# Optimization experiments

Hardware: AMD Instinct MI355X
Metric: run time of the kernel (lower is better)

Reference implementation:

```python
import jax, jax.numpy as jnp
import numpy as np

N, D, H, K, C = 8192, 1024, 512, 16, 9  # patches, embed, hidden, heads, classes


def setup_inputs() -> dict:
    key = jax.random.key(0)
    ks = jax.random.split(key, 20)
    sD = 1.0 / np.sqrt(D)
    sH = 1.0 / np.sqrt(H)
    inp = {
        "x": jax.random.normal(ks[0], (N, D), jnp.float32),
        # gated attention heads, stacked over K heads; weights stored [in, out]
        "Vw": jax.random.normal(ks[1], (K, D, H), jnp.float32) * sD,
        "Vb": jax.random.normal(ks[2], (K, H), jnp.float32) * sD,
        "Uw": jax.random.normal(ks[3], (K, D, H), jnp.float32) * sD,
        "Ub": jax.random.normal(ks[4], (K, H), jnp.float32) * sD,
        "ww": jax.random.normal(ks[5], (K, H), jnp.float32) * sH,
        "wb": jax.random.normal(ks[6], (K,), jnp.float32) * sH,
        # average-pooling head MLP: D -> H -> D
        "pW1": jax.random.normal(ks[7], (D, H), jnp.float32) * sD,
        "pb1": jax.random.normal(ks[8], (H,), jnp.float32) * sD,
        "pW2": jax.random.normal(ks[9], (H, D), jnp.float32) * sH,
        "pb2": jax.random.normal(ks[10], (D,), jnp.float32) * sH,
        # classifier: D -> 1024 -> 512 -> 256 -> C
        "cW1": jax.random.normal(ks[11], (D, 1024), jnp.float32) * sD,
        "cb1": jax.random.normal(ks[12], (1024,), jnp.float32) * sD,
        "cW2": jax.random.normal(ks[13], (1024, 512), jnp.float32) * (1.0 / np.sqrt(1024)),
        "cb2": jax.random.normal(ks[14], (512,), jnp.float32) * (1.0 / np.sqrt(1024)),
        "cW3": jax.random.normal(ks[15], (512, 256), jnp.float32) * (1.0 / np.sqrt(512)),
        "cb3": jax.random.normal(ks[16], (256,), jnp.float32) * (1.0 / np.sqrt(512)),
        "cW4": jax.random.normal(ks[17], (256, C), jnp.float32) * (1.0 / np.sqrt(256)),
        "cb4": jax.random.normal(ks[18], (C,), jnp.float32) * (1.0 / np.sqrt(256)),
    }
    return inp


def reference(x, Vw, Vb, Uw, Ub, ww, wb, pW1, pb1, pW2, pb2,
              cW1, cb1, cW2, cb2, cW3, cb3, cW4, cb4):
    # --- multi-head gated attention (all K heads batched) ---
    AV = jnp.tanh(jnp.einsum('nd,kdh->knh', x, Vw) + Vb[:, None, :])          # [K,N,H]
    AU = jax.nn.sigmoid(jnp.einsum('nd,kdh->knh', x, Uw) + Ub[:, None, :])    # [K,N,H]
    scores = jnp.einsum('knh,kh->kn', AV * AU, ww) + wb[:, None]              # [K,N]
    A = jax.nn.softmax(scores, axis=1)                                        # softmax over patches
    agg_heads = jnp.einsum('kn,nd->kd', A, x)                                 # [K,D]
    # --- average pooling head: mean over patches then MLP D->H->D ---
    m = jnp.mean(x, axis=0)
    avg_agg = jax.nn.relu(m @ pW1 + pb1) @ pW2 + pb2                          # [D]
    # --- mean over all K+1 heads ---
    aggregated = (jnp.sum(agg_heads, axis=0) + avg_agg) / (K + 1)             # [D]
    # --- classifier (eval mode: dropout = identity) ---
    h = jax.nn.relu(aggregated @ cW1 + cb1)
    h = jax.nn.relu(h @ cW2 + cb2)
    h = jax.nn.relu(h @ cW3 + cb3)
    logits = h @ cW4 + cb4                                                    # [C]
    # eval mode applies softmax (not self.training branch)
    return jax.nn.softmax(logits, axis=-1)
```

## Files before the change

### kernel.cpp

```cpp
#include <hip/hip_runtime.h>
#include <stdint.h>

#define N_PATCH 8192
#define DIM     1024
#define HID     512
#define NHEAD   16

using i32x4 = __attribute__((ext_vector_type(4))) int;

__device__ __forceinline__ void gload_lds16(const void* g, void* l) {
  __builtin_amdgcn_global_load_lds(
      reinterpret_cast<const __attribute__((address_space(1))) void*>(
          reinterpret_cast<uintptr_t>(g)),
      reinterpret_cast<__attribute__((address_space(3))) void*>(
          reinterpret_cast<uintptr_t>(l)),
      16, 0, 0);
}

__device__ __forceinline__ int q8(float v, float rs) {
  int q = (int)rintf(v * rs);
  return q > 127 ? 127 : (q < -127 ? -127 : q);
}

__global__ void prep1_kernel(const float* __restrict__ x,
                             signed char* __restrict__ xq, float* __restrict__ sx,
                             const float* __restrict__ Vw, const float* __restrict__ Uw,
                             float* __restrict__ swp, float* __restrict__ rswp) {
  __shared__ __align__(16) float red4[16][16][4];
  const int bid = blockIdx.x;
  const int t = threadIdx.x;
  if (bid < 2048) {
    const int row = bid * 4 + (t >> 6);
    const int lane = t & 63;
    const float* xr = x + (size_t)row * DIM;
    float4 v[4];
    float am = 0.f;
    #pragma unroll
    for (int j = 0; j < 4; ++j) {
      v[j] = *(const float4*)&xr[j * 256 + lane * 4];
      am = fmaxf(am, fmaxf(fmaxf(fabsf(v[j].x), fabsf(v[j].y)),
                           fmaxf(fabsf(v[j].z), fabsf(v[j].w))));
    }
    #pragma unroll
    for (int s = 32; s; s >>= 1) am = fmaxf(am, __shfl_xor(am, s, 64));
    const float rs = (am > 0.f) ? 127.f / am : 0.f;
    #pragma unroll
    for (int j = 0; j < 4; ++j) {
      int b = (q8(v[j].x, rs) & 255) | ((q8(v[j].y, rs) & 255) << 8) |
              ((q8(v[j].z, rs) & 255) << 16) | ((q8(v[j].w, rs) & 255) << 24);
      ((int*)xq)[row * 256 + j * 64 + lane] = b;
    }
    if (lane == 0) sx[row] = am / 127.f;
    return;
  }
  const int b2 = bid - 2048;
  const int u = b2 >> 7, k = (b2 >> 3) & 15, hc = b2 & 7;
  const float* W = u ? Uw : Vw;
  const int h4 = t & 15, dseg = t >> 4;
  const size_t base = (size_t)k * DIM * HID + hc * 64 + h4 * 4;
  float4 am4 = {0.f, 0.f, 0.f, 0.f};
  for (int i = 0; i < 64; ++i) {
    float4 v = *(const float4*)&W[base + (size_t)(dseg * 64 + i) * HID];
    am4.x = fmaxf(am4.x, fabsf(v.x));
    am4.y = fmaxf(am4.y, fabsf(v.y));
    am4.z = fmaxf(am4.z, fabsf(v.z));
    am4.w = fmaxf(am4.w, fabsf(v.w));
  }
  *(float4*)&red4[dseg][h4][0] = am4;
  __syncthreads();
  if (t < 64) {
    float m = 0.f;
    #pragma unroll
    for (int ds = 0; ds < 16; ++ds) m = fmaxf(m, red4[ds][t >> 2][t & 3]);
    const int h = hc * 64 + t;
    const int c = (h >> 4) * 32 + u * 16 + (h & 15);
    swp[k * 1024 + c]  = m / 127.f;
    rswp[k * 1024 + c] = (m > 0.f) ? 127.f / m : 0.f;
  }
}

__global__ void pack_wq_kernel(const float* __restrict__ Vw,
                               const float* __restrict__ Uw,
                               const float* __restrict__ rswp,
                               signed char* __restrict__ Wq) {
  __shared__ __align__(16) signed char T[128][80];
  const int bid = blockIdx.x;
  const int k = bid >> 7, hc = (bid >> 4) & 7, dc = bid & 15;
  const int t = threadIdx.x;
  const int d0 = dc * 64, h0 = hc * 64;
  const int hh = t & 63;
  const size_t base = (size_t)k * DIM * HID;
  #pragma unroll
  for (int u = 0; u < 2; ++u) {
    const float* W = u ? Uw : Vw;
    const int h = h0 + hh;
    const int cl = ((hh >> 4) << 5) + (u << 4) + (hh & 15);
    const float rs = rswp[k * 1024 + hc * 128 + cl];
    #pragma unroll
    for (int i = 0; i < 16; ++i) {
      const int dd = i * 4 + (t >> 6);
      T[cl][dd] = (signed char)q8(W[base + (size_t)(d0 + dd) * HID + h], rs);
    }
  }
  __syncthreads();
  #pragma unroll
  for (int j = 0; j < 2; ++j) {
    const int idx = j * 256 + t;
    const int cl = idx >> 2, dq = idx & 3;
    i32x4 val = *(const i32x4*)&T[cl][dq * 16];
    const size_t col = (size_t)k * 1024 + hc * 128 + cl;
    *(i32x4*)&Wq[col * DIM + d0 + dq * 16] = val;
  }
}

__global__ __launch_bounds__(512, 1) void gemm_scores_kernel(
    const signed char* __restrict__ xq, const signed char* __restrict__ Wq,
    const float* __restrict__ sx, const float* __restrict__ swp,
    const float* __restrict__ Vb, const float* __restrict__ Ub,
    const float* __restrict__ ww, float* __restrict__ part) {
  __shared__ __align__(16) signed char As[2][32768];
  __shared__ __align__(16) signed char Bs[2][32768];
  const int bid = blockIdx.x;
  const int x8 = bid & 7;
  const int s  = (bid >> 3) & 31;
  const int w  = bid >> 8;
  const int mt = (x8 & 1) * 16 + (w & 1) * 8 + (s >> 2);
  const int ct = (x8 >> 1) * 16 + (w >> 1) * 4 + (s & 3);
  const int kh = ct >> 2, cb = ct & 3;
  const int tid = threadIdx.x;
  const int wv = tid >> 6, lane = tid & 63;
  const int wr = wv >> 2, wc = wv & 3;
  const int l15 = lane & 15, l4 = lane >> 4;

  const signed char* Ab = xq + (size_t)mt * 256 * DIM;
  const signed char* Bb = Wq + (size_t)ct * 256 * DIM;

  i32x4 acc[8][4];
  #pragma unroll
  for (int i = 0; i < 8; ++i)
    #pragma unroll
    for (int j = 0; j < 4; ++j) acc[i][j] = (i32x4){0, 0, 0, 0};

  auto stageA_h = [&](int t, int half) {
    const int buf = t & 1, db = t << 7;
    #pragma unroll
    for (int pp = 0; pp < 2; ++pp) {
      const int p = half * 2 + pp;
      const int r = p * 64 + (tid >> 3);
      const int ksrc = ((tid & 7) * 16) ^ (((r >> 1) & 7) << 4);
      gload_lds16(Ab + (size_t)r * DIM + db + ksrc,
                  (char*)&As[buf][0] + p * 8192 + wv * 1024);
    }
  };
  auto stageB_h = [&](int t, int half) {
    const int buf = t & 1, db = t << 7;
    #pragma unroll
    for (int pp = 0; pp < 2; ++pp) {
      const int p = half * 2 + pp;
      const int r = p * 64 + (tid >> 3);
      const int ksrc = ((tid & 7) * 16) ^ (((r >> 1) & 7) << 4);
      gload_lds16(Bb + (size_t)r * DIM + db + ksrc,
                  (char*)&Bs[buf][0] + p * 8192 + wv * 1024);
    }
  };

  const int swz = ((l15 >> 1) & 7) << 4;
  const int kb0 = (0 * 64 + l4 * 16) ^ swz;
  const int kb1 = (1 * 64 + l4 * 16) ^ swz;
  const int aRow = (wr * 128 + l15) * 128;
  const int bRow = (wc * 64 + l15) * 128;

  i32x4 a[8], b[4], a2[8], b2[4];

  stageA_h(0, 0); stageA_h(0, 1); stageB_h(0, 0); stageB_h(0, 1);
  stageA_h(1, 0); stageA_h(1, 1); stageB_h(1, 0); stageB_h(1, 1);
  __syncthreads();

  for (int u = 0; u < 8; ++u) {
    const int buf = u & 1;
    const char* Abase = (const char*)&As[buf][0];
    const char* Bbase = (const char*)&Bs[buf][0];
    #pragma unroll
    for (int f = 0; f < 8; ++f) a[f] = *(const i32x4*)(Abase + aRow + f * 2048 + kb0);
    #pragma unroll
    for (int nf = 0; nf < 4; ++nf) b[nf] = *(const i32x4*)(Bbase + bRow + nf * 2048 + kb0);
    if (u < 7) { stageA_h(u + 1, 0); stageB_h(u + 1, 0); }
    #pragma unroll
    for (int f = 0; f < 8; ++f) a2[f] = *(const i32x4*)(Abase + aRow + f * 2048 + kb1);
    #pragma unroll
    for (int nf = 0; nf < 4; ++nf) b2[nf] = *(const i32x4*)(Bbase + bRow + nf * 2048 + kb1);
    __builtin_amdgcn_s_setprio(1);
    #pragma unroll
    for (int f = 0; f < 8; ++f)
      #pragma unroll
      for (int nf = 0; nf < 4; ++nf)
        acc[f][nf] = __builtin_amdgcn_mfma_i32_16x16x64_i8(a[f], b[nf], acc[f][nf], 0, 0, 0);
    __builtin_amdgcn_s_setprio(0);
    if (u < 7) { stageA_h(u + 1, 1); stageB_h(u + 1, 1); }
    __builtin_amdgcn_s_setprio(1);
    #pragma unroll
    for (int f = 0; f < 8; ++f)
      #pragma unroll
      for (int nf = 0; nf < 4; ++nf)
        acc[f][nf] = __builtin_amdgcn_mfma_i32_16x16x64_i8(a2[f], b2[nf], acc[f][nf], 0, 0, 0);
    __builtin_amdgcn_s_setprio(0);
    __syncthreads();
  }

  float partial[8][4];
  #pragma unroll
  for (int f = 0; f < 8; ++f)
    #pragma unroll
    for (int r = 0; r < 4; ++r) partial[f][r] = 0.f;

  float vb[2], ub[2], wwv[2], swv[2], swu[2];
  #pragma unroll
  for (int p = 0; p < 2; ++p) {
    const int hl = (cb * 8 + wc * 2 + p) * 16 + l15;
    vb[p]  = Vb[kh * HID + hl];
    ub[p]  = Ub[kh * HID + hl];
    wwv[p] = ww[kh * HID + hl];
    swv[p] = swp[ct * 256 + wc * 64 + (2 * p) * 16 + l15];
    swu[p] = swp[ct * 256 + wc * 64 + (2 * p + 1) * 16 + l15];
  }
  const int rbase = mt * 256 + wr * 128 + l4 * 4;
  #pragma unroll
  for (int f = 0; f < 8; ++f) {
    const float4 sx4 = *(const float4*)&sx[rbase + f * 16];
    const float sxr[4] = {sx4.x, sx4.y, sx4.z, sx4.w};
    #pragma unroll
    for (int p = 0; p < 2; ++p)
      #pragma unroll
      for (int r = 0; r < 4; ++r) {
        const float scv = (float)acc[f][2 * p][r] * (sxr[r] * swv[p]) + vb[p];
        const float scu = (float)acc[f][2 * p + 1][r] * (sxr[r] * swu[p]) + ub[p];
        const float e2 = __expf(2.f * scv);
        const float av = 1.f - 2.f / (e2 + 1.f);
        const float au = 1.f / (1.f + __expf(-scu));
        partial[f][r] += av * au * wwv[p];
      }
  }
  #pragma unroll
  for (int s2 = 1; s2 < 16; s2 <<= 1)
    #pragma unroll
    for (int f = 0; f < 8; ++f)
      #pragma unroll
      for (int r = 0; r < 4; ++r)
        partial[f][r] += __shfl_xor(partial[f][r], s2, 64);

  float* red = (float*)&As[0][0];
  if (l15 == 0) {
    #pragma unroll
    for (int f = 0; f < 8; ++f)
      #pragma unroll
      for (int r = 0; r < 4; ++r)
        red[(wr * 4 + wc) * 128 + f * 16 + l4 * 4 + r] = partial[f][r];
  }
  __syncthreads();
  if (tid < 256) {
    const int row = tid;
    const int wr2 = row >> 7, lr = row & 127;
    const float* rp = red + wr2 * 4 * 128;
    const float v = rp[lr] + rp[128 + lr] + rp[256 + lr] + rp[384 + lr];
    part[((size_t)cb * NHEAD + kh) * N_PATCH + mt * 256 + row] = v;
  }
}

__global__ void scores_part_kernel(const float* __restrict__ part,
                                   float* __restrict__ scores,
                                   float* __restrict__ spart) {
  const int k = blockIdx.x >> 3, c = blockIdx.x & 7;
  const int t = threadIdx.x;
  __shared__ float shm[4], shs[4];
  float v[4];
  float mx = -1e30f;
  #pragma unroll
  for (int i = 0; i < 4; ++i) {
    const int n = c * 1024 + i * 256 + t;
    float s = 0.f;
    #pragma unroll
    for (int j = 0; j < 4; ++j) s += part[((size_t)j * NHEAD + k) * N_PATCH + n];
    v[i] = s;
    scores[(size_t)k * N_PATCH + n] = s;
    mx = fmaxf(mx, s);
  }
  #pragma unroll
  for (int sft = 32; sft; sft >>= 1) mx = fmaxf(mx, __shfl_xor(mx, sft, 64));
  const int wv = t >> 6;
  if ((t & 63) == 0) shm[wv] = mx;
  __syncthreads();
  mx = fmaxf(fmaxf(shm[0], shm[1]), fmaxf(shm[2], shm[3]));
  float sum = 0.f;
  #pragma unroll
  for (int i = 0; i < 4; ++i) sum += __expf(v[i] - mx);
  #pragma unroll
  for (int sft = 32; sft; sft >>= 1) sum += __shfl_xor(sum, sft, 64);
  if ((t & 63) == 0) shs[wv] = sum;
  __syncthreads();
  if (t == 0) {
    spart[(k * 8 + c) * 2]     = mx;
    spart[(k * 8 + c) * 2 + 1] = shs[0] + shs[1] + shs[2] + shs[3];
  }
}

__global__ void weighted_part_kernel(const signed char* __restrict__ xq,
                                     const float* __restrict__ sx,
                                     const float* __restrict__ scores,
                                     const float* __restrict__ spart,
                                     float* __restrict__ wp1,
                                     float* __restrict__ wp2) {
  __shared__ float wsx[128], s2x[128];
  __shared__ float sm[16], srz[16];
  const int d = blockIdx.x * 256 + threadIdx.x;
  const int nc = blockIdx.y;
  if (threadIdx.x < 16) {
    const int k = threadIdx.x;
    float m = -1e30f;
    #pragma unroll
    for (int c = 0; c < 8; ++c) m = fmaxf(m, spart[(k * 8 + c) * 2]);
    float S = 0.f;
    #pragma unroll
    for (int c = 0; c < 8; ++c)
      S += spart[(k * 8 + c) * 2 + 1] * __expf(spart[(k * 8 + c) * 2] - m);
    sm[k] = m; srz[k] = 1.f / S;
  }
  __syncthreads();
  if (threadIdx.x < 128) {
    const int n = nc * 128 + threadIdx.x;
    float s = 0.f;
    #pragma unroll
    for (int k = 0; k < NHEAD; ++k)
      s += __expf(scores[(size_t)k * N_PATCH + n] - sm[k]) * srz[k];
    const float sxn = sx[n];
    wsx[threadIdx.x] = s * sxn;
    s2x[threadIdx.x] = sxn;
  }
  __syncthreads();
  float a1 = 0.f, a2 = 0.f;
  for (int i = 0; i < 128; ++i) {
    const float q = (float)xq[(size_t)(nc * 128 + i) * DIM + d];
    a1 += wsx[i] * q;
    a2 += s2x[i] * q;
  }
  wp1[nc * DIM + d] = a1;
  wp2[nc * DIM + d] = a2;
}

__global__ void reduce_vec_kernel(const float* __restrict__ wp1,
                                  const float* __restrict__ wp2,
                                  float* __restrict__ y1,
                                  float* __restrict__ mvec) {
  int d = blockIdx.x * 256 + threadIdx.x;
  float s1 = 0.f, s2 = 0.f;
  #pragma unroll
  for (int i = 0; i < 64; ++i) {
    s1 += wp1[i * DIM + d];
    s2 += wp2[i * DIM + d];
  }
  y1[d] = s1;
  mvec[d] = s2 * (1.f / (float)N_PATCH);
}

__global__ void gemv_fused_kernel(const float* __restrict__ in,
                                  const float* __restrict__ W,
                                  const float* __restrict__ bias,
                                  const float* __restrict__ extra, float scale,
                                  int do_relu, float* __restrict__ out,
                                  int In, int Out) {
  __shared__ float red[4][64];
  const int jl = threadIdx.x & 63, kc = threadIdx.x >> 6;
  const int j = blockIdx.x * 64 + jl;
  const int chunk = In >> 2;
  const float* Wp = W + (size_t)(kc * chunk) * Out + j;
  const float* ip = in + kc * chunk;
  float acc = 0.f;
  #pragma unroll 4
  for (int d = 0; d < chunk; ++d) acc += ip[d] * Wp[(size_t)d * Out];
  if (kc) red[kc][jl] = acc;
  __syncthreads();
  if (kc == 0) {
    float v = bias[j] + acc + red[1][jl] + red[2][jl] + red[3][jl];
    if (extra) v += extra[j];
    v *= scale;
    if (do_relu) v = fmaxf(v, 0.f);
    out[j] = v;
  }
}

__global__ void c3_final_kernel(const float* __restrict__ c2,
                                const float* __restrict__ W3,
                                const float* __restrict__ b3,
                                const float* __restrict__ W4,
                                const float* __restrict__ b4,
                                float* __restrict__ out) {
  __shared__ float c3s[256];
  __shared__ float logits[9];
  const int t = threadIdx.x;
  float acc = b3[t];
  #pragma unroll 4
  for (int d = 0; d < 512; ++d) acc += c2[d] * W3[(size_t)d * 256 + t];
  c3s[t] = fmaxf(acc, 0.f);
  __syncthreads();
  if (t < 9) {
    float l = b4[t];
    for (int d = 0; d < 256; ++d) l += c3s[d] * W4[d * 9 + t];
    logits[t] = l;
  }
  __syncthreads();
  if (t == 0) {
    float mx = logits[0];
    for (int j = 1; j < 9; ++j) mx = fmaxf(mx, logits[j]);
    float e[9], s = 0.f;
    for (int j = 0; j < 9; ++j) { e[j] = expf(logits[j] - mx); s += e[j]; }
    for (int j = 0; j < 9; ++j) out[j] = e[j] / s;
  }
}

extern "C" void kernel_launch(void* const* d_in, const int* in_sizes, int n_in,
                              void* d_out, int out_size, void* d_ws, size_t ws_size,
                              hipStream_t stream) {
  (void)in_sizes; (void)n_in; (void)out_size; (void)ws_size;
  const float* x   = (const float*)d_in[0];
  const float* Vw  = (const float*)d_in[1];
  const float* Vb  = (const float*)d_in[2];
  const float* Uw  = (const float*)d_in[3];
  const float* Ub  = (const float*)d_in[4];
  const float* ww  = (const float*)d_in[5];
  const float* pW1 = (const float*)d_in[7];
  const float* pb1 = (const float*)d_in[8];
  const float* pW2 = (const float*)d_in[9];
  const float* pb2 = (const float*)d_in[10];
  const float* cW1 = (const float*)d_in[11];
  const float* cb1 = (const float*)d_in[12];
  const float* cW2 = (const float*)d_in[13];
  const float* cb2 = (const float*)d_in[14];
  const float* cW3 = (const float*)d_in[15];
  const float* cb3 = (const float*)d_in[16];
  const float* cW4 = (const float*)d_in[17];
  const float* cb4 = (const float*)d_in[18];
  float* out = (float*)d_out;

  char* ws = (char*)d_ws;
  size_t o = 0;
  auto alloc = [&](size_t bytes) -> char* {
    char* p = ws + o;
    o += (bytes + 255) & ~(size_t)255;
    return p;
  };
  signed char* xq = (signed char*)alloc((size_t)N_PATCH * DIM);
  signed char* Wq = (signed char*)alloc((size_t)NHEAD * 1024 * DIM);
  float* sx    = (float*)alloc(N_PATCH * 4);
  float* swp   = (float*)alloc(NHEAD * 1024 * 4);
  float* rswp  = (float*)alloc(NHEAD * 1024 * 4);
  float* part  = (float*)alloc((size_t)4 * NHEAD * N_PATCH * 4);
  float* scores= (float*)alloc((size_t)NHEAD * N_PATCH * 4);
  float* spart = (float*)alloc(NHEAD * 8 * 2 * 4);
  float* wp1   = (float*)alloc(64 * DIM * 4);
  float* wp2   = (float*)alloc(64 * DIM * 4);
  float* y1    = (float*)alloc(DIM * 4);
  float* mvec  = (float*)alloc(DIM * 4);
  float* h1    = (float*)alloc(HID * 4);
  float* aggr  = (float*)alloc(DIM * 4);
  float* c1    = (float*)alloc(1024 * 4);
  float* c2    = (float*)alloc(512 * 4);

  prep1_kernel<<<2304, 256, 0, stream>>>(x, xq, sx, Vw, Uw, swp, rswp);
  pack_wq_kernel<<<2048, 256, 0, stream>>>(Vw, Uw, rswp, Wq);
  gemm_scores_kernel<<<2048, 512, 0, stream>>>(xq, Wq, sx, swp, Vb, Ub, ww, part);
  scores_part_kernel<<<128, 256, 0, stream>>>(part, scores, spart);
  weighted_part_kernel<<<dim3(4, 64), 256, 0, stream>>>(xq, sx, scores, spart, wp1, wp2);
  reduce_vec_kernel<<<4, 256, 0, stream>>>(wp1, wp2, y1, mvec);
  gemv_fused_kernel<<<8, 256, 0, stream>>>(mvec, pW1, pb1, nullptr, 1.f, 1, h1, DIM, HID);
  gemv_fused_kernel<<<16, 256, 0, stream>>>(h1, pW2, pb2, y1, 1.f / 17.f, 0, aggr, HID, DIM);
  gemv_fused_kernel<<<16, 256, 0, stream>>>(aggr, cW1, cb1, nullptr, 1.f, 1, c1, 1024, 1024);
  gemv_fused_kernel<<<8, 256, 0, stream>>>(c1, cW2, cb2, nullptr, 1.f, 1, c2, 1024, 512);
  c3_final_kernel<<<1, 256, 0, stream>>>(c2, cW3, cb3, cW4, cb4, out);
}
```

Measured before the change: 371.4 us.

## Fuse weight absmax reduction into pack kernel and vectorize weight quantization

The per-column absmax scale computation for Vw/Uw moves out of prep1 and into pack_wq, so each block computes its own scales, keeps the reciprocals in shared memory and then quantizes and transposes the weights. This drops the rswp buffer and the dependency across kernels on it, and pack_wq now reads weights with float4 loads instead of scalar loads. The grid shrinks from 2048 to 256 blocks, each doing more work (re-reading its weight slice twice). That lowers parallelism for the packing step and adds more syncthreads per block.

```diff
diff --git a/kernel.cpp b/kernel.cpp
--- a/kernel.cpp
+++ b/kernel.cpp
@@ -23,93 +23,91 @@
 }
 
 __global__ void prep1_kernel(const float* __restrict__ x,
-                             signed char* __restrict__ xq, float* __restrict__ sx,
-                             const float* __restrict__ Vw, const float* __restrict__ Uw,
-                             float* __restrict__ swp, float* __restrict__ rswp) {
-  __shared__ __align__(16) float red4[16][16][4];
+                             signed char* __restrict__ xq, float* __restrict__ sx) {
   const int bid = blockIdx.x;
   const int t = threadIdx.x;
-  if (bid < 2048) {
-    const int row = bid * 4 + (t >> 6);
-    const int lane = t & 63;
-    const float* xr = x + (size_t)row * DIM;
-    float4 v[4];
-    float am = 0.f;
-    #pragma unroll
-    for (int j = 0; j < 4; ++j) {
-      v[j] = *(const float4*)&xr[j * 256 + lane * 4];
-      am = fmaxf(am, fmaxf(fmaxf(fabsf(v[j].x), fabsf(v[j].y)),
-                           fmaxf(fabsf(v[j].z), fabsf(v[j].w))));
+  const int row = bid * 4 + (t >> 6);
+  const int lane = t & 63;
+  const float* xr = x + (size_t)row * DIM;
+  float4 v[4];
+  float am = 0.f;
+  #pragma unroll
+  for (int j = 0; j < 4; ++j) {
+    v[j] = *(const float4*)&xr[j * 256 + lane * 4];
+    am = fmaxf(am, fmaxf(fmaxf(fabsf(v[j].x), fabsf(v[j].y)),
+                         fmaxf(fabsf(v[j].z), fabsf(v[j].w))));
+  }
+  #pragma unroll
+  for (int s = 32; s; s >>= 1) am = fmaxf(am, __shfl_xor(am, s, 64));
+  const float rs = (am > 0.f) ? 127.f / am : 0.f;
+  #pragma unroll
+  for (int j = 0; j < 4; ++j) {
+    int b = (q8(v[j].x, rs) & 255) | ((q8(v[j].y, rs) & 255) << 8) |
+            ((q8(v[j].z, rs) & 255) << 16) | ((q8(v[j].w, rs) & 255) << 24);
+    ((int*)xq)[row * 256 + j * 64 + lane] = b;
+  }
+  if (lane == 0) sx[row] = am / 127.f;
+}
+
+__global__ void pack_wq_kernel(const float* __restrict__ Vw,
+                               const float* __restrict__ Uw,
+                               float* __restrict__ swp,
+                               signed char* __restrict__ Wq) {
+  __shared__ __align__(16) float redm[16][64];
+  __shared__ float rsL[64];
+  __shared__ __align__(16) signed char T[64][288];
+  const int bid = blockIdx.x;
+  const int u = bid >> 7, k = (bid >> 3) & 15, hc = bid & 7;
+  const float* W = u ? Uw : Vw;
+  const int t = threadIdx.x;
+  const size_t base = (size_t)k * DIM * HID + hc * 64;
+
+  {
+    const int h4 = t & 15, dseg = t >> 4;
+    float4 am4 = {0.f, 0.f, 0.f, 0.f};
+    for (int i = 0; i < 64; ++i) {
+      float4 v = *(const float4*)&W[base + (size_t)(dseg * 64 + i) * HID + h4 * 4];
+      am4.x = fmaxf(am4.x, fabsf(v.x));
+      am4.y = fmaxf(am4.y, fabsf(v.y));
+      am4.z = fmaxf(am4.z, fabsf(v.z));
+      am4.w = fmaxf(am4.w, fabsf(v.w));
     }
-    #pragma unroll
-    for (int s = 32; s; s >>= 1) am = fmaxf(am, __shfl_xor(am, s, 64));
-    const float rs = (am > 0.f) ? 127.f / am : 0.f;
-    #pragma unroll
-    for (int j = 0; j < 4; ++j) {
-      int b = (q8(v[j].x, rs) & 255) | ((q8(v[j].y, rs) & 255) << 8) |
-              ((q8(v[j].z, rs) & 255) << 16) | ((q8(v[j].w, rs) & 255) << 24);
-      ((int*)xq)[row * 256 + j * 64 + lane] = b;
-    }
-    if (lane == 0) sx[row] = am / 127.f;
-    return;
-  }
-  const int b2 = bid - 2048;
-  const int u = b2 >> 7, k = (b2 >> 3) & 15, hc = b2 & 7;
-  const float* W = u ? Uw : Vw;
-  const int h4 = t & 15, dseg = t >> 4;
-  const size_t base = (size_t)k * DIM * HID + hc * 64 + h4 * 4;
-  float4 am4 = {0.f, 0.f, 0.f, 0.f};
-  for (int i = 0; i < 64; ++i) {
-    float4 v = *(const float4*)&W[base + (size_t)(dseg * 64 + i) * HID];
-    am4.x = fmaxf(am4.x, fabsf(v.x));
-    am4.y = fmaxf(am4.y, fabsf(v.y));
-    am4.z = fmaxf(am4.z, fabsf(v.z));
-    am4.w = fmaxf(am4.w, fabsf(v.w));
-  }
-  *(float4*)&red4[dseg][h4][0] = am4;
+    *(float4*)&redm[dseg][h4 * 4] = am4;
+  }
   __syncthreads();
   if (t < 64) {
     float m = 0.f;
     #pragma unroll
-    for (int ds = 0; ds < 16; ++ds) m = fmaxf(m, red4[ds][t >> 2][t & 3]);
-    const int h = hc * 64 + t;
-    const int c = (h >> 4) * 32 + u * 16 + (h & 15);
-    swp[k * 1024 + c]  = m / 127.f;
-    rswp[k * 1024 + c] = (m > 0.f) ? 127.f / m : 0.f;
-  }
-}
-
-__global__ void pack_wq_kernel(const float* __restrict__ Vw,
-                               const float* __restrict__ Uw,
-                               const float* __restrict__ rswp,
-                               signed char* __restrict__ Wq) {
-  __shared__ __align__(16) signed char T[128][80];
-  const int bid = blockIdx.x;
-  const int k = bid >> 7, hc = (bid >> 4) & 7, dc = bid & 15;
-  const int t = threadIdx.x;
-  const int d0 = dc * 64, h0 = hc * 64;
-  const int hh = t & 63;
-  const size_t base = (size_t)k * DIM * HID;
-  #pragma unroll
-  for (int u = 0; u < 2; ++u) {
-    const float* W = u ? Uw : Vw;
-    const int h = h0 + hh;
-    const int cl = ((hh >> 4) << 5) + (u << 4) + (hh & 15);
-    const float rs = rswp[k * 1024 + hc * 128 + cl];
+    for (int ds = 0; ds < 16; ++ds) m = fmaxf(m, redm[ds][t]);
+    const int c = k * 1024 + hc * 128 + ((t >> 4) << 5) + (u << 4) + (t & 15);
+    swp[c] = m / 127.f;
+    rsL[t] = (m > 0.f) ? 127.f / m : 0.f;
+  }
+  __syncthreads();
+
+  const int ch = t & 15, rg = t >> 4;
+  const float rs0 = rsL[ch * 4 + 0], rs1 = rsL[ch * 4 + 1];
+  const float rs2 = rsL[ch * 4 + 2], rs3 = rsL[ch * 4 + 3];
+  for (int c256 = 0; c256 < 4; ++c256) {
     #pragma unroll
     for (int i = 0; i < 16; ++i) {
-      const int dd = i * 4 + (t >> 6);
-      T[cl][dd] = (signed char)q8(W[base + (size_t)(d0 + dd) * HID + h], rs);
+      const int dl = rg * 16 + i;
+      float4 v = *(const float4*)&W[base + (size_t)(c256 * 256 + dl) * HID + ch * 4];
+      T[ch * 4 + 0][dl] = (signed char)q8(v.x, rs0);
+      T[ch * 4 + 1][dl] = (signed char)q8(v.y, rs1);
+      T[ch * 4 + 2][dl] = (signed char)q8(v.z, rs2);
+      T[ch * 4 + 3][dl] = (signed char)q8(v.w, rs3);
     }
-  }
-  __syncthreads();
-  #pragma unroll
-  for (int j = 0; j < 2; ++j) {
-    const int idx = j * 256 + t;
-    const int cl = idx >> 2, dq = idx & 3;
-    i32x4 val = *(const i32x4*)&T[cl][dq * 16];
-    const size_t col = (size_t)k * 1024 + hc * 128 + cl;
-    *(i32x4*)&Wq[col * DIM + d0 + dq * 16] = val;
+    __syncthreads();
+    #pragma unroll
+    for (int j = 0; j < 4; ++j) {
+      const int idx = j * 256 + t;
+      const int hh = idx >> 4, dq = idx & 15;
+      i32x4 val = *(const i32x4*)&T[hh][dq * 16];
+      const size_t c = (size_t)k * 1024 + hc * 128 + ((hh >> 4) << 5) + (u << 4) + (hh & 15);
+      *(i32x4*)&Wq[c * DIM + c256 * 256 + dq * 16] = val;
+    }
+    __syncthreads();
   }
 }
 
@@ -451,7 +449,6 @@
   signed char* Wq = (signed char*)alloc((size_t)NHEAD * 1024 * DIM);
   float* sx    = (float*)alloc(N_PATCH * 4);
   float* swp   = (float*)alloc(NHEAD * 1024 * 4);
-  float* rswp  = (float*)alloc(NHEAD * 1024 * 4);
   float* part  = (float*)alloc((size_t)4 * NHEAD * N_PATCH * 4);
   float* scores= (float*)alloc((size_t)NHEAD * N_PATCH * 4);
   float* spart = (float*)alloc(NHEAD * 8 * 2 * 4);
@@ -464,8 +461,8 @@
   float* c1    = (float*)alloc(1024 * 4);
   float* c2    = (float*)alloc(512 * 4);
 
-  prep1_kernel<<<2304, 256, 0, stream>>>(x, xq, sx, Vw, Uw, swp, rswp);
-  pack_wq_kernel<<<2048, 256, 0, stream>>>(Vw, Uw, rswp, Wq);
+  prep1_kernel<<<2048, 256, 0, stream>>>(x, xq, sx);
+  pack_wq_kernel<<<256, 256, 0, stream>>>(Vw, Uw, swp, Wq);
   gemm_scores_kernel<<<2048, 512, 0, stream>>>(xq, Wq, sx, swp, Vb, Ub, ww, part);
   scores_part_kernel<<<128, 256, 0, stream>>>(part, scores, spart);
   weighted_part_kernel<<<dim3(4, 64), 256, 0, stream>>>(xq, sx, scores, spart, wp1, wp2);
```

Result: no change. 365.0 us (median of 3 runs) (-1.7%).
